# Kernel tuning notes

Measured on AMD Instinct MI355X. Metric: run time of the kernel, lower is better.

The kernel has to match this reference:

```python
import jax, jax.numpy as jnp
import numpy as np

DIM = 768
HEADS = 12
HEAD_DIM = DIM // HEADS
SCALE = HEAD_DIM ** -0.5


def setup_inputs() -> dict:
    key = jax.random.key(0)
    ks = jax.random.split(key, 9)
    B, N, M, C = 4, 1024, 1024, DIM
    std = C ** -0.5
    return {
        "q": jax.random.normal(ks[0], (B, N, C), jnp.float32),
        "k": jax.random.normal(ks[1], (B, M, C), jnp.float32),
        "v": jax.random.normal(ks[2], (B, M, C), jnp.float32),
        "mask": jax.random.uniform(ks[3], (B, N, M), jnp.float32),
        "Wq": jax.random.normal(ks[4], (C, C), jnp.float32) * std,
        "Wk": jax.random.normal(ks[5], (C, C), jnp.float32) * std,
        "Wv": jax.random.normal(ks[6], (C, C), jnp.float32) * std,
        "Wp": jax.random.normal(ks[7], (C, C), jnp.float32) * std,
        "bp": jax.random.normal(ks[8], (C,), jnp.float32) * 0.01,
    }


def reference(q, k, v, mask, Wq, Wk, Wv, Wp, bp):
    B, N, C = q.shape
    M = k.shape[1]
    H, D = HEADS, HEAD_DIM
    qh = (q @ Wq).reshape(B, N, H, D)
    kh = (k @ Wk).reshape(B, M, H, D)
    vh = (v @ Wv).reshape(B, M, H, D)
    attn = jnp.einsum('bnhd,bmhd->bhnm', qh, kh) * SCALE
    attn = jax.nn.softmax(attn, axis=-1)
    # post-softmax multiplicative mask, broadcast over heads
    attn = attn * mask[:, None, :, :]
    x = jnp.einsum('bhnm,bmhd->bnhd', attn, vh).reshape(B, N, C)
    return x @ Wp + bp
```

## Files before the change

kernel.cpp:

```cpp
#include <hip/hip_runtime.h>

typedef __bf16 bf16x8 __attribute__((ext_vector_type(8)));
typedef float f32x4 __attribute__((ext_vector_type(4)));

__device__ __forceinline__ unsigned short f2bf(float f) {
  union { float f; unsigned u; } x; x.f = f;
  unsigned r = x.u + 0x7FFFu + ((x.u >> 16) & 1u);
  return (unsigned short)(r >> 16);
}

__device__ __forceinline__ void gload_lds16(const void* g, void* l) {
  __builtin_amdgcn_global_load_lds(
      (const __attribute__((address_space(1))) unsigned int*)g,
      (__attribute__((address_space(3))) unsigned int*)l, 16, 0, 0);
}

__device__ __forceinline__ f32x4 mfma16(bf16x8 a, bf16x8 b, f32x4 c) {
  return __builtin_amdgcn_mfma_f32_16x16x32_bf16(a, b, c, 0, 0, 0);
}

__device__ __forceinline__ bf16x8 pack8(const f32x4& a, const f32x4& b) {
  bf16x8 r;
  r[0] = (__bf16)a[0]; r[1] = (__bf16)a[1]; r[2] = (__bf16)a[2]; r[3] = (__bf16)a[3];
  r[4] = (__bf16)b[0]; r[5] = (__bf16)b[1]; r[6] = (__bf16)b[2]; r[7] = (__bf16)b[3];
  return r;
}

__global__ __launch_bounds__(256) void conv_qkv(const float* __restrict__ q,
                                                const float* __restrict__ k,
                                                const float* __restrict__ v,
                                                unsigned short* __restrict__ dst) {
  const float* src = (blockIdx.y == 0) ? q : (blockIdx.y == 1 ? k : v);
  size_t i = ((size_t)blockIdx.x * 256 + threadIdx.x) * 4;
  float4 f = *(const float4*)(src + i);
  ushort4 u;
  u.x = f2bf(f.x); u.y = f2bf(f.y); u.z = f2bf(f.z); u.w = f2bf(f.w);
  *(ushort4*)(dst + (size_t)blockIdx.y * (4096u * 768u) + i) = u;
}

__global__ __launch_bounds__(256) void conv_w(const float* __restrict__ W0,
                                              const float* __restrict__ W1,
                                              const float* __restrict__ W2,
                                              const float* __restrict__ W3,
                                              unsigned short* __restrict__ Wt) {
  __shared__ float tile[32][33];
  const float* W = (blockIdx.z == 0) ? W0 : (blockIdx.z == 1) ? W1
                   : (blockIdx.z == 2) ? W2 : W3;
  int tx = threadIdx.x, ty = threadIdx.y;
  int n0 = blockIdx.x * 32, k0 = blockIdx.y * 32;
#pragma unroll
  for (int i = 0; i < 4; ++i)
    tile[ty * 4 + i][tx] = W[(size_t)(k0 + ty * 4 + i) * 768 + n0 + tx];
  __syncthreads();
  unsigned short* o = Wt + (size_t)blockIdx.z * 768 * 768;
#pragma unroll
  for (int i = 0; i < 4; ++i)
    o[(size_t)(n0 + ty * 4 + i) * 768 + k0 + tx] = f2bf(tile[tx][ty * 4 + i]);
}

__device__ __forceinline__ void gemm_core(const unsigned short* __restrict__ A,
                                          const unsigned short* __restrict__ B,
                                          unsigned short (*As)[64 * 64],
                                          unsigned short (*Bs)[128 * 64],
                                          int m0, int n0, int wm, int wn,
                                          int t, int g, int c16,
                                          f32x4 (&acc)[2][4]) {
  auto stageA = [&](unsigned short* dst, int k0) {
#pragma unroll
    for (int i = 0; i < 2; ++i) {
      int fc = i * 256 + t, r = fc >> 3, c = (fc & 7) ^ ((r >> 1) & 7);
      gload_lds16(A + (size_t)(m0 + r) * 768 + k0 + c * 8, (char*)dst + fc * 16);
    }
  };
  auto stageB = [&](unsigned short* dst, int k0) {
#pragma unroll
    for (int i = 0; i < 4; ++i) {
      int fc = i * 256 + t, r = fc >> 3, c = (fc & 7) ^ ((r >> 1) & 7);
      gload_lds16(B + (size_t)(n0 + r) * 768 + k0 + c * 8, (char*)dst + fc * 16);
    }
  };
  stageA(As[0], 0);
  stageB(Bs[0], 0);
  asm volatile("s_waitcnt vmcnt(0)" ::: "memory");
  __syncthreads();
  for (int s = 0; s < 12; ++s) {
    const int cur = s & 1;
    if (s < 11) {
      stageA(As[cur ^ 1], (s + 1) * 64);
      stageB(Bs[cur ^ 1], (s + 1) * 64);
    }
#pragma unroll
    for (int kk = 0; kk < 2; ++kk) {
      const int ch = kk * 4 + g;
      bf16x8 a[2], bw[4];
#pragma unroll
      for (int mi = 0; mi < 2; ++mi) {
        int r = wm + mi * 16 + c16;
        a[mi] = *(const bf16x8*)((char*)As[cur] + r * 128 + (((ch ^ (r >> 1)) & 7) << 4));
      }
#pragma unroll
      for (int ni = 0; ni < 4; ++ni) {
        int r = wn + ni * 16 + c16;
        bw[ni] = *(const bf16x8*)((char*)Bs[cur] + r * 128 + (((ch ^ (r >> 1)) & 7) << 4));
      }
#pragma unroll
      for (int mi = 0; mi < 2; ++mi)
#pragma unroll
        for (int ni = 0; ni < 4; ++ni)
          acc[mi][ni] = mfma16(a[mi], bw[ni], acc[mi][ni]);
    }
    __syncthreads();
  }
}

__global__ __launch_bounds__(256) void gemm_qkv(const unsigned short* __restrict__ Abase,
                                                const unsigned short* __restrict__ Wt,
                                                unsigned short* __restrict__ Hq,
                                                unsigned short* __restrict__ Hk,
                                                unsigned short* __restrict__ Hvt) {
  __shared__ unsigned short As[2][64 * 64], Bs[2][128 * 64];
  const int flat = blockIdx.x;
  const int lid = (flat & 7) * 144 + (flat >> 3);
  const int z = lid / 384;
  const int rem = lid - z * 384;
  const int m0 = (rem & 63) * 64;
  const int n0 = (rem >> 6) * 128;
  const unsigned short* A = Abase + (size_t)z * 4096 * 768;
  const unsigned short* B = Wt + (size_t)z * 768 * 768;
  const int t = threadIdx.x, l = t & 63, wid = t >> 6;
  const int g = l >> 4, c16 = l & 15;
  const int wm = (wid >> 1) * 32, wn = (wid & 1) * 64;
  f32x4 acc[2][4] = {};
  gemm_core(A, B, As, Bs, m0, n0, wm, wn, t, g, c16, acc);
  if (z < 2) {
    const float f = (z == 0) ? 0.125f * 1.44269504088896341f : 1.0f;
    unsigned short* C = (z == 0) ? Hq : Hk;
#pragma unroll
    for (int mi = 0; mi < 2; ++mi)
#pragma unroll
      for (int ni = 0; ni < 4; ++ni) {
        int col = n0 + wn + ni * 16 + c16;
        int row = m0 + wm + mi * 16 + g * 4;
#pragma unroll
        for (int j = 0; j < 4; ++j)
          C[(size_t)(row + j) * 768 + col] = f2bf(acc[mi][ni][j] * f);
      }
  } else {
#pragma unroll
    for (int mi = 0; mi < 2; ++mi) {
      int rowbase = m0 + wm + mi * 16;
      int bat = rowbase >> 10;
      int mloc = (rowbase & 1023) + g * 4;
#pragma unroll
      for (int ni = 0; ni < 4; ++ni) {
        int col = n0 + wn + ni * 16 + c16;
        ushort4 u;
        u.x = f2bf(acc[mi][ni][0]); u.y = f2bf(acc[mi][ni][1]);
        u.z = f2bf(acc[mi][ni][2]); u.w = f2bf(acc[mi][ni][3]);
        *(ushort4*)(Hvt + (((size_t)(bat * 768 + col)) << 10) + mloc) = u;
      }
    }
  }
}

__global__ __launch_bounds__(256) void attn(const unsigned short* __restrict__ qh,
                                            const unsigned short* __restrict__ kh,
                                            const unsigned short* __restrict__ vhT,
                                            const float* __restrict__ mask,
                                            unsigned short* __restrict__ xb) {
  __shared__ unsigned short Ks[3][64 * 64], Vts[3][64 * 64];
  const int flat = blockIdx.x;
  const int lid = (flat & 7) * 96 + (flat >> 3);
  const int h = lid % 12, qt = (lid / 12) & 15, b = lid / 192;
  const int t = threadIdx.x, l = t & 63, wid = t >> 6;
  const int g = l >> 4, c16 = l & 15;

  const unsigned short* qp =
      qh + ((size_t)(b * 1024 + qt * 64 + wid * 16 + c16)) * 768 + h * 64 + g * 8;
  bf16x8 aq0 = *(const bf16x8*)qp;
  bf16x8 aq1 = *(const bf16x8*)(qp + 32);

  const int fc0 = t, r0 = fc0 >> 3, c0 = (fc0 & 7) ^ ((r0 >> 1) & 7);
  const int fc1 = 256 + t, r1 = fc1 >> 3, c1 = (fc1 & 7) ^ ((r1 >> 1) & 7);
  const int s0 = 32 * (r0 >> 5) + 8 * ((r0 >> 2) & 3) + 4 * ((r0 >> 4) & 1) + (r0 & 3);
  const int s1 = 32 * (r1 >> 5) + 8 * ((r1 >> 2) & 3) + 4 * ((r1 >> 4) & 1) + (r1 & 3);
  const unsigned short* kp0 = kh + (size_t)(b * 1024 + s0) * 768 + h * 64 + c0 * 8;
  const unsigned short* kp1 = kh + (size_t)(b * 1024 + s1) * 768 + h * 64 + c1 * 8;
  const unsigned short* vp0 = vhT + ((size_t)(b * 768 + h * 64 + r0)) * 1024 + c0 * 8;
  const unsigned short* vp1 = vhT + ((size_t)(b * 768 + h * 64 + r1)) * 1024 + c1 * 8;

  auto stageKV = [&](int buf) {
    char* kd = (char*)Ks[buf];
    char* vd = (char*)Vts[buf];
    gload_lds16(kp0, kd + fc0 * 16);
    gload_lds16(kp1, kd + fc1 * 16);
    gload_lds16(vp0, vd + fc0 * 16);
    gload_lds16(vp1, vd + fc1 * 16);
    kp0 += 64 * 768; kp1 += 64 * 768; vp0 += 64; vp1 += 64;
  };

  const float* mq = mask + ((size_t)(b * 1024 + qt * 64 + wid * 16 + c16)) * 1024 + 8 * g;

  stageKV(0);
  stageKV(1);
  asm volatile("s_waitcnt vmcnt(4)" ::: "memory");
  __builtin_amdgcn_s_barrier();

  f32x4 o[4] = {};
  f32x4 ls = {0.f, 0.f, 0.f, 0.f};

  for (int kv = 0; kv < 16; ++kv) {
    const int cur = kv % 3;
    const float* mk = mq + kv * 64;
    f32x4 mreg[4];
    mreg[0] = *(const f32x4*)(mk);
    mreg[1] = *(const f32x4*)(mk + 4);
    mreg[2] = *(const f32x4*)(mk + 32);
    mreg[3] = *(const f32x4*)(mk + 36);
    __builtin_amdgcn_sched_barrier(0);
    if (kv < 14) stageKV((kv + 2) % 3);
    f32x4 p[4] = {};
#pragma unroll
    for (int kk = 0; kk < 2; ++kk) {
      const int ch = kk * 4 + g;
      bf16x8 aq = kk ? aq1 : aq0;
#pragma unroll
      for (int ni = 0; ni < 4; ++ni) {
        int r = ni * 16 + c16;
        bf16x8 bk = *(const bf16x8*)((char*)Ks[cur] + r * 128 + (((ch ^ (r >> 1)) & 7) << 4));
        p[ni] = mfma16(bk, aq, p[ni]);
      }
    }
#pragma unroll
    for (int ni = 0; ni < 4; ++ni) {
      float e0 = exp2f(p[ni][0]);
      float e1 = exp2f(p[ni][1]);
      float e2 = exp2f(p[ni][2]);
      float e3 = exp2f(p[ni][3]);
      ls[ni] += (e0 + e1) + (e2 + e3);
      p[ni][0] = e0 * mreg[ni][0];
      p[ni][1] = e1 * mreg[ni][1];
      p[ni][2] = e2 * mreg[ni][2];
      p[ni][3] = e3 * mreg[ni][3];
    }
    bf16x8 pa0 = pack8(p[0], p[1]);
    bf16x8 pa1 = pack8(p[2], p[3]);
#pragma unroll
    for (int kk = 0; kk < 2; ++kk) {
      const int ch = kk * 4 + g;
      bf16x8 ap = kk ? pa1 : pa0;
#pragma unroll
      for (int ni = 0; ni < 4; ++ni) {
        int r = ni * 16 + c16;
        bf16x8 bv = *(const bf16x8*)((char*)Vts[cur] + r * 128 + (((ch ^ (r >> 1)) & 7) << 4));
        o[ni] = mfma16(ap, bv, o[ni]);
      }
    }
    if (kv < 15) {
      asm volatile("s_waitcnt vmcnt(4)" ::: "memory");
      __builtin_amdgcn_s_barrier();
    }
  }

  float s = (ls[0] + ls[1]) + (ls[2] + ls[3]);
  s += __shfl_xor(s, 16);
  s += __shfl_xor(s, 32);
  float rinv = 1.0f / s;
  const int rb = (l & 48) | ((l >> 2) & 12);
  float rj[4];
#pragma unroll
  for (int j = 0; j < 4; ++j) rj[j] = __shfl(rinv, rb + j);
#pragma unroll
  for (int ni = 0; ni < 4; ++ni) {
    int col = h * 64 + ni * 16 + c16;
    int row = qt * 64 + wid * 16 + g * 4;
#pragma unroll
    for (int j = 0; j < 4; ++j)
      xb[((size_t)(b * 1024) + row + j) * 768 + col] = f2bf(o[ni][j] * rj[j]);
  }
}

__global__ __launch_bounds__(256) void gemm_proj(const unsigned short* __restrict__ A,
                                                 const unsigned short* __restrict__ B,
                                                 const float* __restrict__ bias,
                                                 float* __restrict__ C) {
  __shared__ unsigned short As[2][64 * 64], Bs[2][128 * 64];
  const int flat = blockIdx.x;
  const int lid = (flat & 7) * 48 + (flat >> 3);
  const int m0 = (lid & 63) * 64;
  const int n0 = (lid >> 6) * 128;
  const int t = threadIdx.x, l = t & 63, wid = t >> 6;
  const int g = l >> 4, c16 = l & 15;
  const int wm = (wid >> 1) * 32, wn = (wid & 1) * 64;
  f32x4 acc[2][4] = {};
  gemm_core(A, B, As, Bs, m0, n0, wm, wn, t, g, c16, acc);
#pragma unroll
  for (int mi = 0; mi < 2; ++mi)
#pragma unroll
    for (int ni = 0; ni < 4; ++ni) {
      int col = n0 + wn + ni * 16 + c16;
      int row = m0 + wm + mi * 16 + g * 4;
      float bv = bias[col];
#pragma unroll
      for (int j = 0; j < 4; ++j)
        C[(size_t)(row + j) * 768 + col] = acc[mi][ni][j] + bv;
    }
}

extern "C" void kernel_launch(void* const* d_in, const int* in_sizes, int n_in,
                              void* d_out, int out_size, void* d_ws, size_t ws_size,
                              hipStream_t stream) {
  const float* q    = (const float*)d_in[0];
  const float* k    = (const float*)d_in[1];
  const float* v    = (const float*)d_in[2];
  const float* mask = (const float*)d_in[3];
  const float* Wq   = (const float*)d_in[4];
  const float* Wk   = (const float*)d_in[5];
  const float* Wv   = (const float*)d_in[6];
  const float* Wp   = (const float*)d_in[7];
  const float* bp   = (const float*)d_in[8];
  float* out = (float*)d_out;

  const size_t MN = (size_t)4096 * 768;
  const size_t WW = (size_t)768 * 768;
  unsigned short* qkv_bf = (unsigned short*)d_ws;
  unsigned short* wt     = qkv_bf + 3 * MN;
  unsigned short* heads  = wt + 4 * WW;
  unsigned short* xb     = heads + 3 * MN;

  conv_qkv<<<dim3(3072, 3), 256, 0, stream>>>(q, k, v, qkv_bf);
  conv_w<<<dim3(24, 24, 4), dim3(32, 8), 0, stream>>>(Wq, Wk, Wv, Wp, wt);
  gemm_qkv<<<dim3(1152), 256, 0, stream>>>(qkv_bf, wt, heads, heads + MN, heads + 2 * MN);
  attn<<<dim3(768), 256, 0, stream>>>(heads, heads + MN, heads + 2 * MN, mask, xb);
  gemm_proj<<<dim3(384), 256, 0, stream>>>(xb, wt + 3 * WW, bp, out);
}
```

Measured before the change: 108.0 us.

## Replace LDS-staged attention with single-wave blocks loading K/V fragments directly

The attention kernel drops the triple-buffered LDS staging of K and V shared by four waves. It now launches one 64-thread wave per 16-query tile, and each lane loads its own K/V MFMA fragments straight from global memory into registers. This removes LDS traffic, barriers and the async copy pipeline. In exchange, K/V reuse across the four waves now depends on L2/L1 caching, global load traffic per query row rises, and there is no explicit prefetch to hide load latency.

Result: slower. 171.3 us (+58.7%).

```diff
diff --git a/kernel.cpp b/kernel.cpp
--- a/kernel.cpp
+++ b/kernel.cpp
@@ -163,74 +163,60 @@
   }
 }
 
-__global__ __launch_bounds__(256) void attn(const unsigned short* __restrict__ qh,
-                                            const unsigned short* __restrict__ kh,
-                                            const unsigned short* __restrict__ vhT,
-                                            const float* __restrict__ mask,
-                                            unsigned short* __restrict__ xb) {
-  __shared__ unsigned short Ks[3][64 * 64], Vts[3][64 * 64];
+__global__ __launch_bounds__(64) void attn(const unsigned short* __restrict__ qh,
+                                           const unsigned short* __restrict__ kh,
+                                           const unsigned short* __restrict__ vhT,
+                                           const float* __restrict__ mask,
+                                           unsigned short* __restrict__ xb) {
   const int flat = blockIdx.x;
-  const int lid = (flat & 7) * 96 + (flat >> 3);
-  const int h = lid % 12, qt = (lid / 12) & 15, b = lid / 192;
-  const int t = threadIdx.x, l = t & 63, wid = t >> 6;
+  const int lid = (flat & 7) * 384 + (flat >> 3);
+  const int h = lid % 12;
+  const int r2 = lid / 12;
+  const int qw = r2 & 63, b = r2 >> 6;
+  const int l = threadIdx.x;
   const int g = l >> 4, c16 = l & 15;
 
   const unsigned short* qp =
-      qh + ((size_t)(b * 1024 + qt * 64 + wid * 16 + c16)) * 768 + h * 64 + g * 8;
+      qh + ((size_t)(b * 1024 + qw * 16 + c16)) * 768 + h * 64 + g * 8;
   bf16x8 aq0 = *(const bf16x8*)qp;
   bf16x8 aq1 = *(const bf16x8*)(qp + 32);
 
-  const int fc0 = t, r0 = fc0 >> 3, c0 = (fc0 & 7) ^ ((r0 >> 1) & 7);
-  const int fc1 = 256 + t, r1 = fc1 >> 3, c1 = (fc1 & 7) ^ ((r1 >> 1) & 7);
-  const int s0 = 32 * (r0 >> 5) + 8 * ((r0 >> 2) & 3) + 4 * ((r0 >> 4) & 1) + (r0 & 3);
-  const int s1 = 32 * (r1 >> 5) + 8 * ((r1 >> 2) & 3) + 4 * ((r1 >> 4) & 1) + (r1 & 3);
-  const unsigned short* kp0 = kh + (size_t)(b * 1024 + s0) * 768 + h * 64 + c0 * 8;
-  const unsigned short* kp1 = kh + (size_t)(b * 1024 + s1) * 768 + h * 64 + c1 * 8;
-  const unsigned short* vp0 = vhT + ((size_t)(b * 768 + h * 64 + r0)) * 1024 + c0 * 8;
-  const unsigned short* vp1 = vhT + ((size_t)(b * 768 + h * 64 + r1)) * 1024 + c1 * 8;
-
-  auto stageKV = [&](int buf) {
-    char* kd = (char*)Ks[buf];
-    char* vd = (char*)Vts[buf];
-    gload_lds16(kp0, kd + fc0 * 16);
-    gload_lds16(kp1, kd + fc1 * 16);
-    gload_lds16(vp0, vd + fc0 * 16);
-    gload_lds16(vp1, vd + fc1 * 16);
-    kp0 += 64 * 768; kp1 += 64 * 768; vp0 += 64; vp1 += 64;
-  };
-
-  const float* mq = mask + ((size_t)(b * 1024 + qt * 64 + wid * 16 + c16)) * 1024 + 8 * g;
-
-  stageKV(0);
-  stageKV(1);
-  asm volatile("s_waitcnt vmcnt(4)" ::: "memory");
-  __builtin_amdgcn_s_barrier();
+  const unsigned short* kq[4];
+  const unsigned short* vq[4];
+#pragma unroll
+  for (int ni = 0; ni < 4; ++ni) {
+    int p = ni * 16 + c16;
+    int sr = 32 * (p >> 5) + 8 * ((p >> 2) & 3) + 4 * ((p >> 4) & 1) + (p & 3);
+    kq[ni] = kh + (size_t)(b * 1024 + sr) * 768 + h * 64 + g * 8;
+    vq[ni] = vhT + ((size_t)(b * 768 + h * 64 + p)) * 1024 + g * 8;
+  }
+  const float* mq = mask + ((size_t)(b * 1024 + qw * 16 + c16)) * 1024 + 8 * g;
 
   f32x4 o[4] = {};
   f32x4 ls = {0.f, 0.f, 0.f, 0.f};
 
   for (int kv = 0; kv < 16; ++kv) {
-    const int cur = kv % 3;
-    const float* mk = mq + kv * 64;
+    bf16x8 kf0[4], kf1[4], vf0[4], vf1[4];
+#pragma unroll
+    for (int ni = 0; ni < 4; ++ni) {
+      kf0[ni] = *(const bf16x8*)(kq[ni]);
+      kf1[ni] = *(const bf16x8*)(kq[ni] + 32);
+      vf0[ni] = *(const bf16x8*)(vq[ni]);
+      vf1[ni] = *(const bf16x8*)(vq[ni] + 32);
+      kq[ni] += 64 * 768;
+      vq[ni] += 64;
+    }
     f32x4 mreg[4];
-    mreg[0] = *(const f32x4*)(mk);
-    mreg[1] = *(const f32x4*)(mk + 4);
-    mreg[2] = *(const f32x4*)(mk + 32);
-    mreg[3] = *(const f32x4*)(mk + 36);
-    __builtin_amdgcn_sched_barrier(0);
-    if (kv < 14) stageKV((kv + 2) % 3);
+    mreg[0] = *(const f32x4*)(mq);
+    mreg[1] = *(const f32x4*)(mq + 4);
+    mreg[2] = *(const f32x4*)(mq + 32);
+    mreg[3] = *(const f32x4*)(mq + 36);
+    mq += 64;
     f32x4 p[4] = {};
 #pragma unroll
-    for (int kk = 0; kk < 2; ++kk) {
-      const int ch = kk * 4 + g;
-      bf16x8 aq = kk ? aq1 : aq0;
-#pragma unroll
-      for (int ni = 0; ni < 4; ++ni) {
-        int r = ni * 16 + c16;
-        bf16x8 bk = *(const bf16x8*)((char*)Ks[cur] + r * 128 + (((ch ^ (r >> 1)) & 7) << 4));
-        p[ni] = mfma16(bk, aq, p[ni]);
-      }
-    }
+    for (int ni = 0; ni < 4; ++ni) p[ni] = mfma16(kf0[ni], aq0, p[ni]);
+#pragma unroll
+    for (int ni = 0; ni < 4; ++ni) p[ni] = mfma16(kf1[ni], aq1, p[ni]);
 #pragma unroll
     for (int ni = 0; ni < 4; ++ni) {
       float e0 = exp2f(p[ni][0]);
@@ -246,20 +232,9 @@
     bf16x8 pa0 = pack8(p[0], p[1]);
     bf16x8 pa1 = pack8(p[2], p[3]);
 #pragma unroll
-    for (int kk = 0; kk < 2; ++kk) {
-      const int ch = kk * 4 + g;
-      bf16x8 ap = kk ? pa1 : pa0;
-#pragma unroll
-      for (int ni = 0; ni < 4; ++ni) {
-        int r = ni * 16 + c16;
-        bf16x8 bv = *(const bf16x8*)((char*)Vts[cur] + r * 128 + (((ch ^ (r >> 1)) & 7) << 4));
-        o[ni] = mfma16(ap, bv, o[ni]);
-      }
-    }
-    if (kv < 15) {
-      asm volatile("s_waitcnt vmcnt(4)" ::: "memory");
-      __builtin_amdgcn_s_barrier();
-    }
+    for (int ni = 0; ni < 4; ++ni) o[ni] = mfma16(pa0, vf0[ni], o[ni]);
+#pragma unroll
+    for (int ni = 0; ni < 4; ++ni) o[ni] = mfma16(pa1, vf1[ni], o[ni]);
   }
 
   float s = (ls[0] + ls[1]) + (ls[2] + ls[3]);
@@ -273,7 +248,7 @@
 #pragma unroll
   for (int ni = 0; ni < 4; ++ni) {
     int col = h * 64 + ni * 16 + c16;
-    int row = qt * 64 + wid * 16 + g * 4;
+    int row = qw * 16 + g * 4;
 #pragma unroll
     for (int j = 0; j < 4; ++j)
       xb[((size_t)(b * 1024) + row + j) * 768 + col] = f2bf(o[ni][j] * rj[j]);
@@ -331,6 +306,6 @@
   conv_qkv<<<dim3(3072, 3), 256, 0, stream>>>(q, k, v, qkv_bf);
   conv_w<<<dim3(24, 24, 4), dim3(32, 8), 0, stream>>>(Wq, Wk, Wv, Wp, wt);
   gemm_qkv<<<dim3(1152), 256, 0, stream>>>(qkv_bf, wt, heads, heads + MN, heads + 2 * MN);
-  attn<<<dim3(768), 256, 0, stream>>>(heads, heads + MN, heads + 2 * MN, mask, xb);
+  attn<<<dim3(3072), 64, 0, stream>>>(heads, heads + MN, heads + 2 * MN, mask, xb);
   gemm_proj<<<dim3(384), 256, 0, stream>>>(xb, wt + 3 * WW, bp, out);
 }
```

## Enlarge QKV GEMM tile to 128x128 and simplify attention KV pipeline sync

Applied to the files above, without the earlier changes.

The QKV projection GEMM moves from 64x128 to 128x128 block tiles. Its double-buffered main loop is now inlined, with each wave computing a 4x4 grid of MFMA tiles, and the grid is halved to 576 blocks. The aim is more data reuse per LDS load and fewer blocks. In the attention kernel, KV staging uses explicit offsets instead of advancing pointers, the prefetch is issued before the mask loads, and the loop is fully unrolled. The partial vmcnt(4) wait plus raw barrier is replaced by __syncthreads, which may force a full wait on in-flight prefetches and shorten the effective pipeline depth.

Result: slower. 140.7 us (+30.3%).

```diff
diff --git a/kernel.cpp b/kernel.cpp
--- a/kernel.cpp
+++ b/kernel.cpp
@@ -118,25 +118,65 @@
                                                 unsigned short* __restrict__ Hq,
                                                 unsigned short* __restrict__ Hk,
                                                 unsigned short* __restrict__ Hvt) {
-  __shared__ unsigned short As[2][64 * 64], Bs[2][128 * 64];
+  __shared__ unsigned short As[2][128 * 64], Bs[2][128 * 64];
   const int flat = blockIdx.x;
-  const int lid = (flat & 7) * 144 + (flat >> 3);
-  const int z = lid / 384;
-  const int rem = lid - z * 384;
-  const int m0 = (rem & 63) * 64;
-  const int n0 = (rem >> 6) * 128;
+  const int lid = (flat & 7) * 72 + (flat >> 3);
+  const int z = lid / 192;
+  const int rem = lid - z * 192;
+  const int m0 = (rem & 31) * 128;
+  const int n0 = (rem >> 5) * 128;
   const unsigned short* A = Abase + (size_t)z * 4096 * 768;
   const unsigned short* B = Wt + (size_t)z * 768 * 768;
   const int t = threadIdx.x, l = t & 63, wid = t >> 6;
   const int g = l >> 4, c16 = l & 15;
-  const int wm = (wid >> 1) * 32, wn = (wid & 1) * 64;
-  f32x4 acc[2][4] = {};
-  gemm_core(A, B, As, Bs, m0, n0, wm, wn, t, g, c16, acc);
+  const int wm = (wid >> 1) * 64, wn = (wid & 1) * 64;
+
+  auto stage = [&](unsigned short* dst, const unsigned short* src, int base, int k0) {
+#pragma unroll
+    for (int i = 0; i < 4; ++i) {
+      int fc = i * 256 + t, r = fc >> 3, c = (fc & 7) ^ ((r >> 1) & 7);
+      gload_lds16(src + (size_t)(base + r) * 768 + k0 + c * 8, (char*)dst + fc * 16);
+    }
+  };
+  stage(As[0], A, m0, 0);
+  stage(Bs[0], B, n0, 0);
+  asm volatile("s_waitcnt vmcnt(0)" ::: "memory");
+  __syncthreads();
+  f32x4 acc[4][4] = {};
+  for (int s = 0; s < 12; ++s) {
+    const int cur = s & 1;
+    if (s < 11) {
+      stage(As[cur ^ 1], A, m0, (s + 1) * 64);
+      stage(Bs[cur ^ 1], B, n0, (s + 1) * 64);
+    }
+#pragma unroll
+    for (int kk = 0; kk < 2; ++kk) {
+      const int ch = kk * 4 + g;
+      bf16x8 a[4], bw[4];
+#pragma unroll
+      for (int mi = 0; mi < 4; ++mi) {
+        int r = wm + mi * 16 + c16;
+        a[mi] = *(const bf16x8*)((char*)As[cur] + r * 128 + (((ch ^ (r >> 1)) & 7) << 4));
+      }
+#pragma unroll
+      for (int ni = 0; ni < 4; ++ni) {
+        int r = wn + ni * 16 + c16;
+        bw[ni] = *(const bf16x8*)((char*)Bs[cur] + r * 128 + (((ch ^ (r >> 1)) & 7) << 4));
+      }
+#pragma unroll
+      for (int mi = 0; mi < 4; ++mi)
+#pragma unroll
+        for (int ni = 0; ni < 4; ++ni)
+          acc[mi][ni] = mfma16(a[mi], bw[ni], acc[mi][ni]);
+    }
+    __syncthreads();
+  }
+
   if (z < 2) {
     const float f = (z == 0) ? 0.125f * 1.44269504088896341f : 1.0f;
     unsigned short* C = (z == 0) ? Hq : Hk;
 #pragma unroll
-    for (int mi = 0; mi < 2; ++mi)
+    for (int mi = 0; mi < 4; ++mi)
 #pragma unroll
       for (int ni = 0; ni < 4; ++ni) {
         int col = n0 + wn + ni * 16 + c16;
@@ -147,7 +187,7 @@
       }
   } else {
 #pragma unroll
-    for (int mi = 0; mi < 2; ++mi) {
+    for (int mi = 0; mi < 4; ++mi) {
       int rowbase = m0 + wm + mi * 16;
       int bat = rowbase >> 10;
       int mloc = (rowbase & 1023) + g * 4;
@@ -189,36 +229,34 @@
   const unsigned short* vp0 = vhT + ((size_t)(b * 768 + h * 64 + r0)) * 1024 + c0 * 8;
   const unsigned short* vp1 = vhT + ((size_t)(b * 768 + h * 64 + r1)) * 1024 + c1 * 8;
 
-  auto stageKV = [&](int buf) {
+  auto stageKV = [&](int buf, int kv) {
     char* kd = (char*)Ks[buf];
     char* vd = (char*)Vts[buf];
-    gload_lds16(kp0, kd + fc0 * 16);
-    gload_lds16(kp1, kd + fc1 * 16);
-    gload_lds16(vp0, vd + fc0 * 16);
-    gload_lds16(vp1, vd + fc1 * 16);
-    kp0 += 64 * 768; kp1 += 64 * 768; vp0 += 64; vp1 += 64;
+    gload_lds16(kp0 + (size_t)kv * 64 * 768, kd + fc0 * 16);
+    gload_lds16(kp1 + (size_t)kv * 64 * 768, kd + fc1 * 16);
+    gload_lds16(vp0 + kv * 64, vd + fc0 * 16);
+    gload_lds16(vp1 + kv * 64, vd + fc1 * 16);
   };
 
   const float* mq = mask + ((size_t)(b * 1024 + qt * 64 + wid * 16 + c16)) * 1024 + 8 * g;
 
-  stageKV(0);
-  stageKV(1);
-  asm volatile("s_waitcnt vmcnt(4)" ::: "memory");
-  __builtin_amdgcn_s_barrier();
+  stageKV(0, 0);
+  stageKV(1, 1);
+  __syncthreads();
 
   f32x4 o[4] = {};
   f32x4 ls = {0.f, 0.f, 0.f, 0.f};
 
+#pragma unroll
   for (int kv = 0; kv < 16; ++kv) {
     const int cur = kv % 3;
+    if (kv < 14) stageKV((kv + 2) % 3, kv + 2);
     const float* mk = mq + kv * 64;
     f32x4 mreg[4];
     mreg[0] = *(const f32x4*)(mk);
     mreg[1] = *(const f32x4*)(mk + 4);
     mreg[2] = *(const f32x4*)(mk + 32);
     mreg[3] = *(const f32x4*)(mk + 36);
-    __builtin_amdgcn_sched_barrier(0);
-    if (kv < 14) stageKV((kv + 2) % 3);
     f32x4 p[4] = {};
 #pragma unroll
     for (int kk = 0; kk < 2; ++kk) {
@@ -256,10 +294,7 @@
         o[ni] = mfma16(ap, bv, o[ni]);
       }
     }
-    if (kv < 15) {
-      asm volatile("s_waitcnt vmcnt(4)" ::: "memory");
-      __builtin_amdgcn_s_barrier();
-    }
+    if (kv < 15) __syncthreads();
   }
 
   float s = (ls[0] + ls[1]) + (ls[2] + ls[3]);
@@ -330,7 +365,7 @@
 
   conv_qkv<<<dim3(3072, 3), 256, 0, stream>>>(q, k, v, qkv_bf);
   conv_w<<<dim3(24, 24, 4), dim3(32, 8), 0, stream>>>(Wq, Wk, Wv, Wp, wt);
-  gemm_qkv<<<dim3(1152), 256, 0, stream>>>(qkv_bf, wt, heads, heads + MN, heads + 2 * MN);
+  gemm_qkv<<<dim3(576), 256, 0, stream>>>(qkv_bf, wt, heads, heads + MN, heads + 2 * MN);
   attn<<<dim3(768), 256, 0, stream>>>(heads, heads + MN, heads + 2 * MN, mask, xb);
   gemm_proj<<<dim3(384), 256, 0, stream>>>(xb, wt + 3 * WW, bp, out);
 }
```
